# Performance work log

Measured on AMD Instinct MI355X. Metric: run time of the kernel, lower is better.

The kernel has to match this reference:

```python
import jax, jax.numpy as jnp
import numpy as np

N, S, E, HEADS = 8, 2048, 1024, 16


def setup_inputs() -> dict:
    root = jax.random.key(0)
    k1, k2, k3, k4, k5, k6 = jax.random.split(root, 6)
    query = jax.random.normal(k1, (N, S, E), jnp.float32)
    key_t = jax.random.normal(k2, (N, S, E), jnp.float32)
    value = jax.random.normal(k3, (N, S, E), jnp.float32)
    # mask broadcasts against the (buggy) energy tensor of shape (N, S, H, H)
    mask = jax.random.randint(k4, (1, 1, HEADS, HEADS), 0, 2, jnp.int32)
    # guarantee no all-masked softmax row (avoid NaN)
    diag = jnp.arange(HEADS)
    mask = mask.at[0, 0, diag, diag].set(1)
    W_out = jax.random.normal(k5, (E, E), jnp.float32) / np.float32(np.sqrt(E))
    b_out = jax.random.normal(k6, (E,), jnp.float32) * 0.02
    return {"query": query, "key": key_t, "value": value, "mask": mask,
            "W_out": W_out, "b_out": b_out, "heads": HEADS}


def reference(query, key, value, mask, W_out, b_out, heads):
    # Faithful translation of the original forward, INCLUDING its einsum-label
    # bug: tensors are transposed to (N, H, S, D) but the einsum subscripts
    # treat axis 1 as 'q/k' and axis 2 as 'h', so softmax runs over heads.
    n, q_len, e = query.shape
    d = e // heads
    inv_scale = np.float32(1.0 / np.sqrt(d))
    q = query.reshape(n, q_len, heads, d).transpose(0, 2, 1, 3)   # (N,H,S,D)
    k = key.reshape(n, q_len, heads, d).transpose(0, 2, 1, 3)     # (N,H,S,D)
    v = value.reshape(n, q_len, heads, d).transpose(0, 2, 1, 3)   # (N,H,S,D)
    # labels applied to transposed tensors -> energy shape (N, S, H, H)
    energy = jnp.einsum('nqhd,nkhd->nhqk', q, k) * inv_scale
    energy = jnp.where(mask == 0, -jnp.inf, energy)
    attention = jax.nn.softmax(energy, axis=-1)                   # over heads axis
    out = jnp.einsum('nhql,nlhd->nqhd', attention, v)             # (N,H,S,D)
    out = out.reshape(n, q_len, e)                                # raw memory reinterp, as torch does
    return out @ W_out.T + b_out
```

## Files before the change

kernel.cpp:

```cpp
#include <hip/hip_runtime.h>
#include <stdint.h>

#define S_LEN 2048
#define EMB 1024

typedef __bf16 bf16x8 __attribute__((ext_vector_type(8)));
typedef __bf16 bf16x4 __attribute__((ext_vector_type(4)));
typedef float f32x4 __attribute__((ext_vector_type(4)));

__device__ __forceinline__ unsigned short f2bf(float f) {
  unsigned int b = __float_as_uint(f);
  b += 0x7FFFu + ((b >> 16) & 1u);
  return (unsigned short)(b >> 16);
}

__device__ __forceinline__ bf16x8 cvt8(float4 a, float4 b) {
  bf16x8 r;
  r[0] = (__bf16)a.x; r[1] = (__bf16)a.y; r[2] = (__bf16)a.z; r[3] = (__bf16)a.w;
  r[4] = (__bf16)b.x; r[5] = (__bf16)b.y; r[6] = (__bf16)b.z; r[7] = (__bf16)b.w;
  return r;
}

#define GLD16(gp, lp)                                                          \
  __builtin_amdgcn_global_load_lds(                                            \
      (const __attribute__((address_space(1))) void*)(gp),                     \
      (__attribute__((address_space(3))) void*)(lp), 16, 0, 0)

__global__ __launch_bounds__(256) void attn_kernel(
    const float* __restrict__ Q, const float* __restrict__ K,
    const float* __restrict__ V, const int* __restrict__ mask,
    __bf16* __restrict__ X) {
  __shared__ __bf16 Vb[4][1024];
  __shared__ __bf16 As[4][16][16];

  const int lane = threadIdx.x & 63;
  const int wv = threadIdx.x >> 6;
  const int pos = blockIdx.x * 4 + wv;
  const int n = pos >> 11;
  const int s = pos & 2047;
  const int col = lane & 15;
  const int grp = lane >> 4;
  const int gc = grp & 1;
  const int fo = col * 64 + grp * 8;

  const float* qrow = Q + (size_t)pos * EMB;
  const float* krow = K + (size_t)pos * EMB;
  const float* vrow = V + (size_t)pos * EMB;

  float4 vload[4];
#pragma unroll
  for (int c = 0; c < 4; ++c)
    vload[c] = *(const float4*)(vrow + c * 256 + lane * 4);

  float4 qraw[4], kraw[4];
#pragma unroll
  for (int t = 0; t < 2; ++t) {
    qraw[t * 2 + 0] = *(const float4*)(qrow + fo + t * 32);
    qraw[t * 2 + 1] = *(const float4*)(qrow + fo + t * 32 + 4);
    kraw[t * 2 + 0] = *(const float4*)(krow + fo + t * 32);
    kraw[t * 2 + 1] = *(const float4*)(krow + fo + t * 32 + 4);
  }
  const int4 mrow = *(const int4*)(mask + col * 16 + grp * 4);
  __builtin_amdgcn_sched_barrier(0);

#pragma unroll
  for (int c = 0; c < 4; ++c) {
    bf16x4 w;
    w[0] = (__bf16)vload[c].x;
    w[1] = (__bf16)vload[c].y;
    w[2] = (__bf16)vload[c].z;
    w[3] = (__bf16)vload[c].w;
    *(bf16x4*)&Vb[wv][c * 256 + lane * 4] = w;
  }

  const bf16x8 qa0 = cvt8(qraw[0], qraw[1]);
  const bf16x8 qa1 = cvt8(qraw[2], qraw[3]);
  const bf16x8 kb0 = cvt8(kraw[0], kraw[1]);
  const bf16x8 kb1 = cvt8(kraw[2], kraw[3]);
  f32x4 en = {0.f, 0.f, 0.f, 0.f};
  en = __builtin_amdgcn_mfma_f32_16x16x32_bf16(kb0, qa0, en, 0, 0, 0);
  en = __builtin_amdgcn_mfma_f32_16x16x32_bf16(kb1, qa1, en, 0, 0, 0);

  float p[4];
  p[0] = (mrow.x == 0) ? -1e30f : en[0] * 0.125f;
  p[1] = (mrow.y == 0) ? -1e30f : en[1] * 0.125f;
  p[2] = (mrow.z == 0) ? -1e30f : en[2] * 0.125f;
  p[3] = (mrow.w == 0) ? -1e30f : en[3] * 0.125f;
  float mx = fmaxf(fmaxf(p[0], p[1]), fmaxf(p[2], p[3]));
  mx = fmaxf(mx, __shfl_xor(mx, 16));
  mx = fmaxf(mx, __shfl_xor(mx, 32));
  float ex[4], sm = 0.f;
#pragma unroll
  for (int r = 0; r < 4; ++r) {
    ex[r] = __expf(p[r] - mx);
    sm += ex[r];
  }
  sm += __shfl_xor(sm, 16);
  sm += __shfl_xor(sm, 32);
  const float inv = __builtin_amdgcn_rcpf(sm);
  bf16x4 aw;
#pragma unroll
  for (int r = 0; r < 4; ++r) aw[r] = (__bf16)(ex[r] * inv);
  *(bf16x4*)&As[wv][col][grp * 4] = aw;

  const bf16x8 pt = *(const bf16x8*)&As[wv][col][gc * 8];
  bf16x8 pa;
#pragma unroll
  for (int e = 0; e < 8; ++e) pa[e] = (grp < 2) ? pt[e] : (__bf16)0.f;

  const size_t xrow = (size_t)n * S_LEN + (size_t)col * 128 + (s >> 4);
  __bf16* xp = X + xrow * EMB + (size_t)((s & 15) * 64 + grp * 4);
#pragma unroll
  for (int c = 0; c < 4; ++c) {
    bf16x8 vf;
#pragma unroll
    for (int e = 0; e < 8; ++e)
      vf[e] = Vb[wv][(gc * 8 + e) * 64 + c * 16 + col];
    f32x4 o = {0.f, 0.f, 0.f, 0.f};
    o = __builtin_amdgcn_mfma_f32_16x16x32_bf16(vf, pa, o, 0, 0, 0);
    bf16x4 w;
#pragma unroll
    for (int r = 0; r < 4; ++r) w[r] = (__bf16)o[r];
    *(bf16x4*)(xp + c * 16) = w;
  }
}

__global__ __launch_bounds__(256) void wconv_kernel(
    const float* __restrict__ W, unsigned short* __restrict__ Wb) {
  const int idx = blockIdx.x * 256 + threadIdx.x;
  float4 w = *(const float4*)(W + (size_t)idx * 4);
  ushort4 o;
  o.x = f2bf(w.x);
  o.y = f2bf(w.y);
  o.z = f2bf(w.z);
  o.w = f2bf(w.w);
  *(ushort4*)(Wb + (size_t)idx * 4) = o;
}

__global__ __launch_bounds__(256) void gemm_kernel(
    const unsigned short* __restrict__ A, const unsigned short* __restrict__ B,
    const float* __restrict__ bias, float* __restrict__ C) {
  __shared__ unsigned short sA[128 * 32];
  __shared__ unsigned short sB[128 * 32];

  int bid = blockIdx.x;
  const int cpx = gridDim.x >> 3;
  bid = (bid & 7) * cpx + (bid >> 3);
  const int tileM = (bid >> 3) * 128;
  const int tileN = (bid & 7) * 128;

  const int t = threadIdx.x;
  const int lane = t & 63;
  const int wid = t >> 6;
  const int wm = wid >> 1, wn = wid & 1;
  const int lrow = lane & 15;
  const int lgrp = lane >> 4;

  f32x4 acc[4][4];
#pragma unroll
  for (int a = 0; a < 4; ++a)
#pragma unroll
    for (int b = 0; b < 4; ++b) acc[a][b] = (f32x4){0.f, 0.f, 0.f, 0.f};

  const int row0 = t >> 2;
  const int kk = (t & 3) * 8;
  const size_t abase = ((size_t)(tileM + row0)) * 1024 + kk;
  const size_t bbase = ((size_t)(tileN + row0)) * 1024 + kk;

  for (int k0 = 0; k0 < 1024; k0 += 32) {
#pragma unroll
    for (int c = 0; c < 2; ++c) {
      GLD16(A + abase + (size_t)c * 64 * 1024 + k0,
            (char*)sA + c * 4096 + t * 16);
      GLD16(B + bbase + (size_t)c * 64 * 1024 + k0,
            (char*)sB + c * 4096 + t * 16);
    }
    __syncthreads();

    bf16x8 af[4], bfr[4];
#pragma unroll
    for (int mi = 0; mi < 4; ++mi)
      af[mi] = *(const bf16x8*)&sA[(wm * 64 + mi * 16 + lrow) * 32 + lgrp * 8];
#pragma unroll
    for (int ni = 0; ni < 4; ++ni)
      bfr[ni] = *(const bf16x8*)&sB[(wn * 64 + ni * 16 + lrow) * 32 + lgrp * 8];
#pragma unroll
    for (int mi = 0; mi < 4; ++mi)
#pragma unroll
      for (int ni = 0; ni < 4; ++ni)
        acc[mi][ni] = __builtin_amdgcn_mfma_f32_16x16x32_bf16(
            af[mi], bfr[ni], acc[mi][ni], 0, 0, 0);
    __syncthreads();
  }

#pragma unroll
  for (int ni = 0; ni < 4; ++ni) {
    const int colc = tileN + wn * 64 + ni * 16 + lrow;
    const float bv = bias[colc];
#pragma unroll
    for (int mi = 0; mi < 4; ++mi) {
      const int row = tileM + wm * 64 + mi * 16 + lgrp * 4;
#pragma unroll
      for (int r = 0; r < 4; ++r)
        C[(size_t)(row + r) * 1024 + colc] = acc[mi][ni][r] + bv;
    }
  }
}

extern "C" void kernel_launch(void* const* d_in, const int* in_sizes, int n_in,
                              void* d_out, int out_size, void* d_ws,
                              size_t ws_size, hipStream_t stream) {
  const float* Q = (const float*)d_in[0];
  const float* K = (const float*)d_in[1];
  const float* V = (const float*)d_in[2];
  const int* mask = (const int*)d_in[3];
  const float* W = (const float*)d_in[4];
  const float* bias = (const float*)d_in[5];
  float* out = (float*)d_out;

  __bf16* X = (__bf16*)d_ws;
  unsigned short* Wb =
      (unsigned short*)((char*)d_ws + (size_t)32 * 1024 * 1024);

  hipLaunchKernelGGL(attn_kernel, dim3(8 * S_LEN / 4), dim3(256), 0, stream,
                     Q, K, V, mask, X);
  hipLaunchKernelGGL(wconv_kernel, dim3(1024), dim3(256), 0, stream, W, Wb);
  hipLaunchKernelGGL(gemm_kernel, dim3(1024), dim3(256), 0, stream,
                     (const unsigned short*)X, Wb, bias, out);
}
```

Measured before the change: 100.1 us.

## Process four positions per wave with double-buffered register prefetch in attention

Each wave in the attention kernel now handles four sequence positions instead of one. Loads for the next position are issued into a second register set while the current one is computed, with double-buffered LDS slots. The grid shrinks fourfold. The goal is to hide global-load latency in a memory-bound kernel. The cost is higher register and LDS use and fewer blocks to spread across the GPU.

```diff
diff --git a/kernel.cpp b/kernel.cpp
--- a/kernel.cpp
+++ b/kernel.cpp
@@ -26,57 +26,50 @@
       (const __attribute__((address_space(1))) void*)(gp),                     \
       (__attribute__((address_space(3))) void*)(lp), 16, 0, 0)
 
-__global__ __launch_bounds__(256) void attn_kernel(
-    const float* __restrict__ Q, const float* __restrict__ K,
-    const float* __restrict__ V, const int* __restrict__ mask,
-    __bf16* __restrict__ X) {
-  __shared__ __bf16 Vb[4][1024];
-  __shared__ __bf16 As[4][16][16];
-
-  const int lane = threadIdx.x & 63;
-  const int wv = threadIdx.x >> 6;
-  const int pos = blockIdx.x * 4 + wv;
-  const int n = pos >> 11;
-  const int s = pos & 2047;
-  const int col = lane & 15;
-  const int grp = lane >> 4;
-  const int gc = grp & 1;
-  const int fo = col * 64 + grp * 8;
-
+__device__ __forceinline__ void issue_loads(const float* __restrict__ Q,
+                                            const float* __restrict__ K,
+                                            const float* __restrict__ V,
+                                            int pos, int lane, int fo,
+                                            float4 v[4], float4 q[4],
+                                            float4 k[4]) {
   const float* qrow = Q + (size_t)pos * EMB;
   const float* krow = K + (size_t)pos * EMB;
   const float* vrow = V + (size_t)pos * EMB;
-
-  float4 vload[4];
 #pragma unroll
   for (int c = 0; c < 4; ++c)
-    vload[c] = *(const float4*)(vrow + c * 256 + lane * 4);
-
-  float4 qraw[4], kraw[4];
-#pragma unroll
-  for (int t = 0; t < 2; ++t) {
-    qraw[t * 2 + 0] = *(const float4*)(qrow + fo + t * 32);
-    qraw[t * 2 + 1] = *(const float4*)(qrow + fo + t * 32 + 4);
-    kraw[t * 2 + 0] = *(const float4*)(krow + fo + t * 32);
-    kraw[t * 2 + 1] = *(const float4*)(krow + fo + t * 32 + 4);
-  }
-  const int4 mrow = *(const int4*)(mask + col * 16 + grp * 4);
-  __builtin_amdgcn_sched_barrier(0);
+    v[c] = *(const float4*)(vrow + c * 256 + lane * 4);
+  q[0] = *(const float4*)(qrow + fo);
+  q[1] = *(const float4*)(qrow + fo + 4);
+  q[2] = *(const float4*)(qrow + fo + 32);
+  q[3] = *(const float4*)(qrow + fo + 36);
+  k[0] = *(const float4*)(krow + fo);
+  k[1] = *(const float4*)(krow + fo + 4);
+  k[2] = *(const float4*)(krow + fo + 32);
+  k[3] = *(const float4*)(krow + fo + 36);
+}
+
+__device__ __forceinline__ void compute_pos(
+    int pos, int lane, int col, int grp, int gc, int wv, int slot,
+    const int4 mrow, const float4 v[4], const float4 q[4], const float4 k[4],
+    __bf16 (&Vb)[4][2][1024], __bf16 (&As)[4][2][16][16],
+    __bf16* __restrict__ X) {
+  const int n = pos >> 11;
+  const int s = pos & 2047;
 
 #pragma unroll
   for (int c = 0; c < 4; ++c) {
     bf16x4 w;
-    w[0] = (__bf16)vload[c].x;
-    w[1] = (__bf16)vload[c].y;
-    w[2] = (__bf16)vload[c].z;
-    w[3] = (__bf16)vload[c].w;
-    *(bf16x4*)&Vb[wv][c * 256 + lane * 4] = w;
-  }
-
-  const bf16x8 qa0 = cvt8(qraw[0], qraw[1]);
-  const bf16x8 qa1 = cvt8(qraw[2], qraw[3]);
-  const bf16x8 kb0 = cvt8(kraw[0], kraw[1]);
-  const bf16x8 kb1 = cvt8(kraw[2], kraw[3]);
+    w[0] = (__bf16)v[c].x;
+    w[1] = (__bf16)v[c].y;
+    w[2] = (__bf16)v[c].z;
+    w[3] = (__bf16)v[c].w;
+    *(bf16x4*)&Vb[wv][slot][c * 256 + lane * 4] = w;
+  }
+
+  const bf16x8 qa0 = cvt8(q[0], q[1]);
+  const bf16x8 qa1 = cvt8(q[2], q[3]);
+  const bf16x8 kb0 = cvt8(k[0], k[1]);
+  const bf16x8 kb1 = cvt8(k[2], k[3]);
   f32x4 en = {0.f, 0.f, 0.f, 0.f};
   en = __builtin_amdgcn_mfma_f32_16x16x32_bf16(kb0, qa0, en, 0, 0, 0);
   en = __builtin_amdgcn_mfma_f32_16x16x32_bf16(kb1, qa1, en, 0, 0, 0);
@@ -101,9 +94,9 @@
   bf16x4 aw;
 #pragma unroll
   for (int r = 0; r < 4; ++r) aw[r] = (__bf16)(ex[r] * inv);
-  *(bf16x4*)&As[wv][col][grp * 4] = aw;
-
-  const bf16x8 pt = *(const bf16x8*)&As[wv][col][gc * 8];
+  *(bf16x4*)&As[wv][slot][col][grp * 4] = aw;
+
+  const bf16x8 pt = *(const bf16x8*)&As[wv][slot][col][gc * 8];
   bf16x8 pa;
 #pragma unroll
   for (int e = 0; e < 8; ++e) pa[e] = (grp < 2) ? pt[e] : (__bf16)0.f;
@@ -115,7 +108,7 @@
     bf16x8 vf;
 #pragma unroll
     for (int e = 0; e < 8; ++e)
-      vf[e] = Vb[wv][(gc * 8 + e) * 64 + c * 16 + col];
+      vf[e] = Vb[wv][slot][(gc * 8 + e) * 64 + c * 16 + col];
     f32x4 o = {0.f, 0.f, 0.f, 0.f};
     o = __builtin_amdgcn_mfma_f32_16x16x32_bf16(vf, pa, o, 0, 0, 0);
     bf16x4 w;
@@ -123,6 +116,42 @@
     for (int r = 0; r < 4; ++r) w[r] = (__bf16)o[r];
     *(bf16x4*)(xp + c * 16) = w;
   }
+}
+
+__global__ __launch_bounds__(256) void attn_kernel(
+    const float* __restrict__ Q, const float* __restrict__ K,
+    const float* __restrict__ V, const int* __restrict__ mask,
+    __bf16* __restrict__ X) {
+  __shared__ __bf16 Vb[4][2][1024];
+  __shared__ __bf16 As[4][2][16][16];
+
+  const int lane = threadIdx.x & 63;
+  const int wv = threadIdx.x >> 6;
+  const int pos0 = (blockIdx.x * 4 + wv) * 4;
+  const int col = lane & 15;
+  const int grp = lane >> 4;
+  const int gc = grp & 1;
+  const int fo = col * 64 + grp * 8;
+
+  const int4 mrow = *(const int4*)(mask + col * 16 + grp * 4);
+
+  float4 vA[4], qA[4], kA[4];
+  float4 vB[4], qB[4], kB[4];
+
+  issue_loads(Q, K, V, pos0 + 0, lane, fo, vA, qA, kA);
+  issue_loads(Q, K, V, pos0 + 1, lane, fo, vB, qB, kB);
+  __builtin_amdgcn_sched_barrier(0);
+
+  compute_pos(pos0 + 0, lane, col, grp, gc, wv, 0, mrow, vA, qA, kA, Vb, As, X);
+  issue_loads(Q, K, V, pos0 + 2, lane, fo, vA, qA, kA);
+  __builtin_amdgcn_sched_barrier(0);
+
+  compute_pos(pos0 + 1, lane, col, grp, gc, wv, 1, mrow, vB, qB, kB, Vb, As, X);
+  issue_loads(Q, K, V, pos0 + 3, lane, fo, vB, qB, kB);
+  __builtin_amdgcn_sched_barrier(0);
+
+  compute_pos(pos0 + 2, lane, col, grp, gc, wv, 0, mrow, vA, qA, kA, Vb, As, X);
+  compute_pos(pos0 + 3, lane, col, grp, gc, wv, 1, mrow, vB, qB, kB, Vb, As, X);
 }
 
 __global__ __launch_bounds__(256) void wconv_kernel(
@@ -222,7 +251,7 @@
   unsigned short* Wb =
       (unsigned short*)((char*)d_ws + (size_t)32 * 1024 * 1024);
 
-  hipLaunchKernelGGL(attn_kernel, dim3(8 * S_LEN / 4), dim3(256), 0, stream,
+  hipLaunchKernelGGL(attn_kernel, dim3(8 * S_LEN / 16), dim3(256), 0, stream,
                      Q, K, V, mask, X);
   hipLaunchKernelGGL(wconv_kernel, dim3(1024), dim3(256), 0, stream, W, Wb);
   hipLaunchKernelGGL(gemm_kernel, dim3(1024), dim3(256), 0, stream,
```

New measurement: 99.38 us. No clear change (-0.7%).
